# Performance work log

Measured on AMD Instinct MI355X. Metric: run time of the kernel, lower is better.

## Reference

```python
import jax, jax.numpy as jnp
import numpy as np

NUM_NODES = 1_000_000
H_DIM = 64
OUT_DIM = 32
NUM_RELS = 64
NUM_BASES = 4
N_SRC0 = 400_000
N_DST1 = 100_000
N_DST2 = 20_000
E1 = 600_000
E2 = 300_000


def setup_inputs() -> dict:
    key = jax.random.key(0)
    ks = jax.random.split(key, 16)
    inp = {
        "input_nodes": jax.random.randint(ks[0], (N_SRC0,), 0, NUM_NODES),
        "src1": jax.random.randint(ks[1], (E1,), 0, N_SRC0),
        "dst1": jax.random.randint(ks[2], (E1,), 0, N_DST1),
        "etype1": jax.random.randint(ks[3], (E1,), 0, NUM_RELS),
        "norm1": jax.random.uniform(ks[4], (E1, 1), dtype=jnp.float32),
        "src2": jax.random.randint(ks[5], (E2,), 0, N_DST1),
        "dst2": jax.random.randint(ks[6], (E2,), 0, N_DST2),
        "etype2": jax.random.randint(ks[7], (E2,), 0, NUM_RELS),
        "norm2": jax.random.uniform(ks[8], (E2, 1), dtype=jnp.float32),
        # learned parameters
        "emb": jax.random.normal(ks[9], (NUM_NODES, H_DIM), dtype=jnp.float32),
        "V1": jax.random.normal(ks[10], (NUM_BASES, H_DIM, H_DIM), dtype=jnp.float32) * 0.05,
        "comp1": jax.random.normal(ks[11], (NUM_RELS, NUM_BASES), dtype=jnp.float32) * 0.3,
        "b1": jnp.zeros((H_DIM,), dtype=jnp.float32),
        "V2": jax.random.normal(ks[12], (NUM_BASES, H_DIM, OUT_DIM), dtype=jnp.float32) * 0.05,
        "comp2": jax.random.normal(ks[13], (NUM_RELS, NUM_BASES), dtype=jnp.float32) * 0.3,
        "b2": jnp.zeros((OUT_DIM,), dtype=jnp.float32),
    }
    return inp


def rel_graph_conv(x, src, dst, etype, norm, V, comp, bias, n_dst):
    """Basis-decomposed RelGraphConv (no self-loop): m_e = (x[src_e] @ W_{etype_e}) * norm_e,
    with W_r = sum_b comp[r,b] V[b]; aggregate by sum into dst nodes, then add bias."""
    xe = x[src]                                 # [E, d] gather of source features
    coeff = comp[etype]                         # [E, B] relation coefficients per edge
    y = jnp.einsum('ed,bdo->ebo', xe, V)        # [E, B, o] feature x each basis
    m = jnp.einsum('ebo,eb->eo', y, coeff)      # [E, o] relation-specific message
    m = m * norm                                # per-edge normalization ([E,1] broadcast)
    h = jax.ops.segment_sum(m, dst, num_segments=n_dst)  # scatter-add to dst
    return h + bias


def reference(input_nodes, src1, dst1, etype1, norm1, src2, dst2, etype2, norm2,
              emb, V1, comp1, b1, V2, comp2, b2):
    x = emb[input_nodes]                                           # [N_src0, h]
    h = rel_graph_conv(x, src1, dst1, etype1, norm1, V1, comp1, b1, N_DST1)
    h = jax.nn.relu(h)
    out = rel_graph_conv(h, src2, dst2, etype2, norm2, V2, comp2, b2, N_DST2)
    return out
```

## Files before the change

kernel.cpp:

```cpp
#include <hip/hip_runtime.h>
#include <stdint.h>

#define NUM_NODES 1000000
#define H_DIM 64
#define OUT_DIM 32
#define NUM_RELS 64
#define NUM_BASES 4
#define N_SRC0 400000
#define N_DST1 100000
#define N_DST2 20000
#define E1 600000
#define E2 300000
#define NDST_TOT (N_DST1 + N_DST2)
#define E_TOT (E1 + E2)

typedef __attribute__((ext_vector_type(8))) short bf16x8;
typedef __attribute__((ext_vector_type(4))) float floatx4;

__device__ __forceinline__ unsigned short f2bf(float f){
  union{float f; unsigned u;} v; v.f=f;
  unsigned u=v.u;
  unsigned r=(u + 0x7FFFu + ((u>>16)&1u))>>16;
  return (unsigned short)r;
}
__device__ __forceinline__ float bf2f(unsigned short h){
  union{unsigned u; float f;} v; v.u=((unsigned)h)<<16; return v.f;
}

__global__ void k_init(const float* __restrict__ V1, const float* __restrict__ V2,
                       ushort* __restrict__ Btab1, ushort* __restrict__ Btab2,
                       int* __restrict__ deg){
  int t = blockIdx.x*blockDim.x + threadIdx.x;
  if (t < NDST_TOT) deg[t] = 0;
  if (t < 16384){
    int j = t & 7, lane = (t>>3)&63, kk = (t>>9)&7, nt = t>>12;
    int kdim = kk*32 + (lane>>4)*8 + j;
    int o = nt*16 + (lane&15);
    int k = kdim>>2, b = kdim&3;
    Btab1[t] = f2bf(V1[(b*64 + k)*64 + o]);
  } else if (t < 24576){
    int u = t - 16384;
    int j = u & 7, lane = (u>>3)&63, kk = (u>>9)&7, nt = u>>12;
    int kdim = kk*32 + (lane>>4)*8 + j;
    int o = nt*16 + (lane&15);
    int k = kdim>>2, b = kdim&3;
    Btab2[u] = f2bf(V2[(b*64 + k)*32 + o]);
  }
}

__global__ void k_hist(const int* __restrict__ dst1, const int* __restrict__ dst2,
                       int* __restrict__ deg){
  int t = blockIdx.x*blockDim.x + threadIdx.x;
  if (t < E1) atomicAdd(&deg[dst1[t]], 1);
  else if (t < E_TOT) atomicAdd(&deg[N_DST1 + dst2[t - E1]], 1);
}

__global__ void k_scan_sum(const int* __restrict__ deg, int* __restrict__ bsum, int n){
  __shared__ int lds[256];
  int tid = threadIdx.x;
  int base = blockIdx.x*1024 + tid*4;
  int s = 0;
  #pragma unroll
  for (int j=0;j<4;j++){ int i = base+j; if (i<n) s += deg[i]; }
  lds[tid] = s; __syncthreads();
  for (int off=128; off>0; off>>=1){ if (tid<off) lds[tid] += lds[tid+off]; __syncthreads(); }
  if (tid==0) bsum[blockIdx.x] = lds[0];
}

__global__ void k_scan_bsum(const int* __restrict__ bsum, int* __restrict__ boff, int nb){
  __shared__ int lds[256];
  int tid = threadIdx.x;
  int v = (tid<nb) ? bsum[tid] : 0;
  lds[tid] = v; __syncthreads();
  for (int off=1; off<256; off<<=1){
    int t = (tid>=off) ? lds[tid-off] : 0; __syncthreads();
    lds[tid] += t; __syncthreads();
  }
  if (tid<nb) boff[tid] = lds[tid] - v;
}

__global__ void k_scan_final(const int* __restrict__ deg, const int* __restrict__ boff,
                             int* __restrict__ offs, int* __restrict__ cursor, int n){
  __shared__ int lds[256];
  int tid = threadIdx.x;
  int base = blockIdx.x*1024 + tid*4;
  int a[4]; int s = 0;
  #pragma unroll
  for (int j=0;j<4;j++){ int i = base+j; a[j] = (i<n)?deg[i]:0; s += a[j]; }
  lds[tid] = s; __syncthreads();
  for (int off=1; off<256; off<<=1){
    int t = (tid>=off) ? lds[tid-off] : 0; __syncthreads();
    lds[tid] += t; __syncthreads();
  }
  int run = boff[blockIdx.x] + (lds[tid] - s);
  #pragma unroll
  for (int j=0;j<4;j++){
    int i = base+j;
    if (i<n){
      offs[i] = run; cursor[i] = run;
      run += a[j];
      if (i == n-1) offs[n] = run;
    }
  }
}

__global__ void k_scatter(const int* __restrict__ input_nodes,
                          const int* __restrict__ src1, const int* __restrict__ dst1,
                          const int* __restrict__ ety1, const float* __restrict__ nrm1,
                          const float* __restrict__ comp1,
                          const int* __restrict__ src2, const int* __restrict__ dst2,
                          const int* __restrict__ ety2, const float* __restrict__ nrm2,
                          const float* __restrict__ comp2,
                          int* __restrict__ cursor, int* __restrict__ ssrc,
                          float4* __restrict__ sc){
  int t = blockIdx.x*blockDim.x + threadIdx.x;
  int d, s, et; float nv; const float* comp;
  if (t < E1){
    d = dst1[t]; s = input_nodes[src1[t]]; et = ety1[t]; nv = nrm1[t]; comp = comp1;
  } else if (t < E_TOT){
    int e = t - E1;
    d = N_DST1 + dst2[e]; s = src2[e]; et = ety2[e]; nv = nrm2[e]; comp = comp2;
  } else return;
  int p = atomicAdd(&cursor[d], 1);
  ssrc[p] = s;
  float4 cp = ((const float4*)comp)[et];
  float4 c; c.x = cp.x*nv; c.y = cp.y*nv; c.z = cp.z*nv; c.w = cp.w*nv;
  sc[p] = c;
}


__global__ __launch_bounds__(1024) void k_agg_gemm1(
    const float* __restrict__ emb, const int* __restrict__ offs,
    const int* __restrict__ ssrc, const float4* __restrict__ sc,
    const ushort* __restrict__ Btab, const float* __restrict__ bias,
    ushort* __restrict__ h_bf){
  __shared__ ushort zt[16][264];
  int lane = threadIdx.x & 63;
  int w = threadIdx.x >> 6;
  int mbase = blockIdx.x * 16;
  int d = mbase + w;
  int e0 = offs[d], e1 = offs[d+1];
  float a0=0.f, a1=0.f, a2=0.f, a3=0.f;
  int elast = e1 - 1;
  for (int e = e0; e < e1; e += 4){
    int i0 = e,            i1 = min(e+1, elast);
    int i2 = min(e+2, elast), i3 = min(e+3, elast);
    int s0 = ssrc[i0], s1 = ssrc[i1], s2 = ssrc[i2], s3 = ssrc[i3];
    float4 c0 = sc[i0], c1 = sc[i1], c2 = sc[i2], c3 = sc[i3];
    if (e+1 > elast){ c1.x=0.f;c1.y=0.f;c1.z=0.f;c1.w=0.f; }
    if (e+2 > elast){ c2.x=0.f;c2.y=0.f;c2.z=0.f;c2.w=0.f; }
    if (e+3 > elast){ c3.x=0.f;c3.y=0.f;c3.z=0.f;c3.w=0.f; }
    float x0 = emb[(size_t)s0*64 + lane];
    float x1 = emb[(size_t)s1*64 + lane];
    float x2 = emb[(size_t)s2*64 + lane];
    float x3 = emb[(size_t)s3*64 + lane];
    a0 = fmaf(c0.x, x0, a0); a1 = fmaf(c0.y, x0, a1);
    a2 = fmaf(c0.z, x0, a2); a3 = fmaf(c0.w, x0, a3);
    a0 = fmaf(c1.x, x1, a0); a1 = fmaf(c1.y, x1, a1);
    a2 = fmaf(c1.z, x1, a2); a3 = fmaf(c1.w, x1, a3);
    a0 = fmaf(c2.x, x2, a0); a1 = fmaf(c2.y, x2, a1);
    a2 = fmaf(c2.z, x2, a2); a3 = fmaf(c2.w, x2, a3);
    a0 = fmaf(c3.x, x3, a0); a1 = fmaf(c3.y, x3, a1);
    a2 = fmaf(c3.z, x3, a2); a3 = fmaf(c3.w, x3, a3);
  }
  ushort4 o; o.x=f2bf(a0); o.y=f2bf(a1); o.z=f2bf(a2); o.w=f2bf(a3);
  *(ushort4*)&zt[w][lane*4] = o;
  __syncthreads();
  if (w >= 4) return;
  int quad = lane>>4, l15 = lane&15;
  bf16x8 a[8];
  #pragma unroll
  for (int kk=0; kk<8; kk++)
    a[kk] = *(const bf16x8*)&zt[l15][kk*32 + quad*8];
  floatx4 acc = {0.f,0.f,0.f,0.f};
  #pragma unroll
  for (int kk=0; kk<8; kk++){
    bf16x8 b = *((const bf16x8*)(Btab + ((w*8 + kk)*64 + lane)*8));
    acc = __builtin_amdgcn_mfma_f32_16x16x32_bf16(a[kk], b, acc, 0, 0, 0);
  }
  int col = w*16 + l15;
  float bv = bias[col];
  #pragma unroll
  for (int r=0; r<4; r++){
    int row = mbase + quad*4 + r;
    float v = fmaxf(acc[r] + bv, 0.f);
    h_bf[(size_t)row*64 + col] = f2bf(v);
  }
}

__global__ __launch_bounds__(1024) void k_agg_gemm2(
    const ushort* __restrict__ hin, const int* __restrict__ offs,
    const int* __restrict__ ssrc, const float4* __restrict__ sc,
    const ushort* __restrict__ Btab, const float* __restrict__ bias,
    float* __restrict__ out){
  __shared__ ushort zt[16][264];
  int lane = threadIdx.x & 63;
  int w = threadIdx.x >> 6;
  int mbase = blockIdx.x * 16;
  int d = mbase + w;
  int e0 = offs[d], e1 = offs[d+1];
  float a0=0.f, a1=0.f, a2=0.f, a3=0.f;
  int elast = e1 - 1;
  for (int e = e0; e < e1; e += 4){
    int i0 = e,            i1 = min(e+1, elast);
    int i2 = min(e+2, elast), i3 = min(e+3, elast);
    int s0 = ssrc[i0], s1 = ssrc[i1], s2 = ssrc[i2], s3 = ssrc[i3];
    float4 c0 = sc[i0], c1 = sc[i1], c2 = sc[i2], c3 = sc[i3];
    if (e+1 > elast){ c1.x=0.f;c1.y=0.f;c1.z=0.f;c1.w=0.f; }
    if (e+2 > elast){ c2.x=0.f;c2.y=0.f;c2.z=0.f;c2.w=0.f; }
    if (e+3 > elast){ c3.x=0.f;c3.y=0.f;c3.z=0.f;c3.w=0.f; }
    float x0 = bf2f(hin[(size_t)s0*64 + lane]);
    float x1 = bf2f(hin[(size_t)s1*64 + lane]);
    float x2 = bf2f(hin[(size_t)s2*64 + lane]);
    float x3 = bf2f(hin[(size_t)s3*64 + lane]);
    a0 = fmaf(c0.x, x0, a0); a1 = fmaf(c0.y, x0, a1);
    a2 = fmaf(c0.z, x0, a2); a3 = fmaf(c0.w, x0, a3);
    a0 = fmaf(c1.x, x1, a0); a1 = fmaf(c1.y, x1, a1);
    a2 = fmaf(c1.z, x1, a2); a3 = fmaf(c1.w, x1, a3);
    a0 = fmaf(c2.x, x2, a0); a1 = fmaf(c2.y, x2, a1);
    a2 = fmaf(c2.z, x2, a2); a3 = fmaf(c2.w, x2, a3);
    a0 = fmaf(c3.x, x3, a0); a1 = fmaf(c3.y, x3, a1);
    a2 = fmaf(c3.z, x3, a2); a3 = fmaf(c3.w, x3, a3);
  }
  ushort4 o; o.x=f2bf(a0); o.y=f2bf(a1); o.z=f2bf(a2); o.w=f2bf(a3);
  *(ushort4*)&zt[w][lane*4] = o;
  __syncthreads();
  if (w >= 2) return;
  int quad = lane>>4, l15 = lane&15;
  bf16x8 a[8];
  #pragma unroll
  for (int kk=0; kk<8; kk++)
    a[kk] = *(const bf16x8*)&zt[l15][kk*32 + quad*8];
  floatx4 acc = {0.f,0.f,0.f,0.f};
  #pragma unroll
  for (int kk=0; kk<8; kk++){
    bf16x8 b = *((const bf16x8*)(Btab + ((w*8 + kk)*64 + lane)*8));
    acc = __builtin_amdgcn_mfma_f32_16x16x32_bf16(a[kk], b, acc, 0, 0, 0);
  }
  int col = w*16 + l15;
  float bv = bias[col];
  #pragma unroll
  for (int r=0; r<4; r++){
    int row = mbase + quad*4 + r;
    out[(size_t)row*32 + col] = acc[r] + bv;
  }
}

extern "C" void kernel_launch(void* const* d_in, const int* in_sizes, int n_in,
                              void* d_out, int out_size, void* d_ws, size_t ws_size,
                              hipStream_t stream){
  const int*   input_nodes = (const int*)  d_in[0];
  const int*   src1  = (const int*)  d_in[1];
  const int*   dst1  = (const int*)  d_in[2];
  const int*   ety1  = (const int*)  d_in[3];
  const float* norm1 = (const float*)d_in[4];
  const int*   src2  = (const int*)  d_in[5];
  const int*   dst2  = (const int*)  d_in[6];
  const int*   ety2  = (const int*)  d_in[7];
  const float* norm2 = (const float*)d_in[8];
  const float* emb   = (const float*)d_in[9];
  const float* V1    = (const float*)d_in[10];
  const float* comp1 = (const float*)d_in[11];
  const float* b1    = (const float*)d_in[12];
  const float* V2    = (const float*)d_in[13];
  const float* comp2 = (const float*)d_in[14];
  const float* b2    = (const float*)d_in[15];
  float* out = (float*)d_out;

  char* p = (char*)d_ws;
  auto alloc = [&](size_t bytes)->char*{
    char* r = p; p += (bytes + 255) & ~(size_t)255; return r;
  };
  ushort* h_bf  = (ushort*)alloc((size_t)N_DST1*64*2);
  ushort* Btab1 = (ushort*)alloc(16384*2);
  ushort* Btab2 = (ushort*)alloc(8192*2);
  int* deg  = (int*)alloc((size_t)NDST_TOT*4);
  int* cur  = (int*)alloc((size_t)NDST_TOT*4);
  int* offs = (int*)alloc((size_t)(NDST_TOT+1)*4);
  int* bs   = (int*)alloc(256*4);
  int* bo   = (int*)alloc(256*4);
  int* ssrc = (int*)alloc((size_t)E_TOT*4);
  float4* sc = (float4*)alloc((size_t)E_TOT*16);

  k_init<<<(NDST_TOT + 255)/256, 256, 0, stream>>>(V1, V2, Btab1, Btab2, deg);
  k_hist<<<(E_TOT + 255)/256, 256, 0, stream>>>(dst1, dst2, deg);
  int nb = (NDST_TOT + 1023)/1024;
  k_scan_sum<<<nb, 256, 0, stream>>>(deg, bs, NDST_TOT);
  k_scan_bsum<<<1, 256, 0, stream>>>(bs, bo, nb);
  k_scan_final<<<nb, 256, 0, stream>>>(deg, bo, offs, cur, NDST_TOT);
  k_scatter<<<(E_TOT + 255)/256, 256, 0, stream>>>(input_nodes,
                                                   src1, dst1, ety1, norm1, comp1,
                                                   src2, dst2, ety2, norm2, comp2,
                                                   cur, ssrc, sc);
  k_agg_gemm1<<<N_DST1/16, 1024, 0, stream>>>(emb, offs, ssrc, sc, Btab1, b1, h_bf);
  k_agg_gemm2<<<N_DST2/16, 1024, 0, stream>>>(h_bf, offs + N_DST1, ssrc, sc, Btab2, b2, out);

  (void)in_sizes; (void)n_in; (void)out_size; (void)ws_size;
}
```

Baseline: 506.9 us.

## Replace three-kernel prefix scan with atomic per-wave bucket allocation

Replaces the three-pass exact prefix scan over destination degrees with a single kernel: each wavefront scans its 64 degrees with shuffles and reserves a contiguous range from a global atomic counter. Buckets are no longer in destination order, so the aggregation kernels now compute each segment end as offset plus degree. The Btab conversion is folded into the histogram kernel and degree zeroing moves to a memset, cutting the launch count. The cost is a loss of edge-segment ordering by destination, which may reduce locality of ssrc/sc reads in the aggregation kernels.

```diff
diff --git a/kernel.cpp b/kernel.cpp
--- a/kernel.cpp
+++ b/kernel.cpp
@@ -27,11 +27,11 @@
   union{unsigned u; float f;} v; v.u=((unsigned)h)<<16; return v.f;
 }
 
-__global__ void k_init(const float* __restrict__ V1, const float* __restrict__ V2,
-                       ushort* __restrict__ Btab1, ushort* __restrict__ Btab2,
-                       int* __restrict__ deg){
+__global__ void k_btab_hist(const float* __restrict__ V1, const float* __restrict__ V2,
+                            ushort* __restrict__ Btab1, ushort* __restrict__ Btab2,
+                            const int* __restrict__ dst1, const int* __restrict__ dst2,
+                            int* __restrict__ deg){
   int t = blockIdx.x*blockDim.x + threadIdx.x;
-  if (t < NDST_TOT) deg[t] = 0;
   if (t < 16384){
     int j = t & 7, lane = (t>>3)&63, kk = (t>>9)&7, nt = t>>12;
     int kdim = kk*32 + (lane>>4)*8 + j;
@@ -46,61 +46,28 @@
     int k = kdim>>2, b = kdim&3;
     Btab2[u] = f2bf(V2[(b*64 + k)*32 + o]);
   }
-}
-
-__global__ void k_hist(const int* __restrict__ dst1, const int* __restrict__ dst2,
-                       int* __restrict__ deg){
-  int t = blockIdx.x*blockDim.x + threadIdx.x;
   if (t < E1) atomicAdd(&deg[dst1[t]], 1);
   else if (t < E_TOT) atomicAdd(&deg[N_DST1 + dst2[t - E1]], 1);
 }
 
-__global__ void k_scan_sum(const int* __restrict__ deg, int* __restrict__ bsum, int n){
-  __shared__ int lds[256];
-  int tid = threadIdx.x;
-  int base = blockIdx.x*1024 + tid*4;
-  int s = 0;
-  #pragma unroll
-  for (int j=0;j<4;j++){ int i = base+j; if (i<n) s += deg[i]; }
-  lds[tid] = s; __syncthreads();
-  for (int off=128; off>0; off>>=1){ if (tid<off) lds[tid] += lds[tid+off]; __syncthreads(); }
-  if (tid==0) bsum[blockIdx.x] = lds[0];
-}
-
-__global__ void k_scan_bsum(const int* __restrict__ bsum, int* __restrict__ boff, int nb){
-  __shared__ int lds[256];
-  int tid = threadIdx.x;
-  int v = (tid<nb) ? bsum[tid] : 0;
-  lds[tid] = v; __syncthreads();
-  for (int off=1; off<256; off<<=1){
-    int t = (tid>=off) ? lds[tid-off] : 0; __syncthreads();
-    lds[tid] += t; __syncthreads();
-  }
-  if (tid<nb) boff[tid] = lds[tid] - v;
-}
-
-__global__ void k_scan_final(const int* __restrict__ deg, const int* __restrict__ boff,
-                             int* __restrict__ offs, int* __restrict__ cursor, int n){
-  __shared__ int lds[256];
-  int tid = threadIdx.x;
-  int base = blockIdx.x*1024 + tid*4;
-  int a[4]; int s = 0;
-  #pragma unroll
-  for (int j=0;j<4;j++){ int i = base+j; a[j] = (i<n)?deg[i]:0; s += a[j]; }
-  lds[tid] = s; __syncthreads();
-  for (int off=1; off<256; off<<=1){
-    int t = (tid>=off) ? lds[tid-off] : 0; __syncthreads();
-    lds[tid] += t; __syncthreads();
-  }
-  int run = boff[blockIdx.x] + (lds[tid] - s);
-  #pragma unroll
-  for (int j=0;j<4;j++){
-    int i = base+j;
-    if (i<n){
-      offs[i] = run; cursor[i] = run;
-      run += a[j];
-      if (i == n-1) offs[n] = run;
-    }
+__global__ void k_alloc(const int* __restrict__ deg, int* __restrict__ offs,
+                        int* __restrict__ cursor, int* __restrict__ counter){
+  int t = blockIdx.x*blockDim.x + threadIdx.x;
+  int lane = threadIdx.x & 63;
+  int d = (t < NDST_TOT) ? deg[t] : 0;
+  int incl = d;
+  #pragma unroll
+  for (int off=1; off<64; off<<=1){
+    int v = __shfl_up(incl, off);
+    if (lane >= off) incl += v;
+  }
+  int total = __shfl(incl, 63);
+  int base = 0;
+  if (lane == 0 && total > 0) base = atomicAdd(counter, total);
+  base = __shfl(base, 0);
+  if (t < NDST_TOT){
+    int o = base + incl - d;
+    offs[t] = o; cursor[t] = o;
   }
 }
 
@@ -131,6 +98,7 @@
 
 __global__ __launch_bounds__(1024) void k_agg_gemm1(
     const float* __restrict__ emb, const int* __restrict__ offs,
+    const int* __restrict__ deg,
     const int* __restrict__ ssrc, const float4* __restrict__ sc,
     const ushort* __restrict__ Btab, const float* __restrict__ bias,
     ushort* __restrict__ h_bf){
@@ -139,11 +107,11 @@
   int w = threadIdx.x >> 6;
   int mbase = blockIdx.x * 16;
   int d = mbase + w;
-  int e0 = offs[d], e1 = offs[d+1];
+  int e0 = offs[d], e1 = e0 + deg[d];
   float a0=0.f, a1=0.f, a2=0.f, a3=0.f;
   int elast = e1 - 1;
   for (int e = e0; e < e1; e += 4){
-    int i0 = e,            i1 = min(e+1, elast);
+    int i0 = e,               i1 = min(e+1, elast);
     int i2 = min(e+2, elast), i3 = min(e+3, elast);
     int s0 = ssrc[i0], s1 = ssrc[i1], s2 = ssrc[i2], s3 = ssrc[i3];
     float4 c0 = sc[i0], c1 = sc[i1], c2 = sc[i2], c3 = sc[i3];
@@ -190,6 +158,7 @@
 
 __global__ __launch_bounds__(1024) void k_agg_gemm2(
     const ushort* __restrict__ hin, const int* __restrict__ offs,
+    const int* __restrict__ deg,
     const int* __restrict__ ssrc, const float4* __restrict__ sc,
     const ushort* __restrict__ Btab, const float* __restrict__ bias,
     float* __restrict__ out){
@@ -198,11 +167,11 @@
   int w = threadIdx.x >> 6;
   int mbase = blockIdx.x * 16;
   int d = mbase + w;
-  int e0 = offs[d], e1 = offs[d+1];
+  int e0 = offs[d], e1 = e0 + deg[d];
   float a0=0.f, a1=0.f, a2=0.f, a3=0.f;
   int elast = e1 - 1;
   for (int e = e0; e < e1; e += 4){
-    int i0 = e,            i1 = min(e+1, elast);
+    int i0 = e,               i1 = min(e+1, elast);
     int i2 = min(e+2, elast), i3 = min(e+3, elast);
     int s0 = ssrc[i0], s1 = ssrc[i1], s2 = ssrc[i2], s3 = ssrc[i3];
     float4 c0 = sc[i0], c1 = sc[i1], c2 = sc[i2], c3 = sc[i3];
@@ -274,26 +243,24 @@
   ushort* h_bf  = (ushort*)alloc((size_t)N_DST1*64*2);
   ushort* Btab1 = (ushort*)alloc(16384*2);
   ushort* Btab2 = (ushort*)alloc(8192*2);
-  int* deg  = (int*)alloc((size_t)NDST_TOT*4);
+  int* deg  = (int*)alloc((size_t)(NDST_TOT+1)*4);
   int* cur  = (int*)alloc((size_t)NDST_TOT*4);
-  int* offs = (int*)alloc((size_t)(NDST_TOT+1)*4);
-  int* bs   = (int*)alloc(256*4);
-  int* bo   = (int*)alloc(256*4);
+  int* offs = (int*)alloc((size_t)NDST_TOT*4);
   int* ssrc = (int*)alloc((size_t)E_TOT*4);
   float4* sc = (float4*)alloc((size_t)E_TOT*16);
-
-  k_init<<<(NDST_TOT + 255)/256, 256, 0, stream>>>(V1, V2, Btab1, Btab2, deg);
-  k_hist<<<(E_TOT + 255)/256, 256, 0, stream>>>(dst1, dst2, deg);
-  int nb = (NDST_TOT + 1023)/1024;
-  k_scan_sum<<<nb, 256, 0, stream>>>(deg, bs, NDST_TOT);
-  k_scan_bsum<<<1, 256, 0, stream>>>(bs, bo, nb);
-  k_scan_final<<<nb, 256, 0, stream>>>(deg, bo, offs, cur, NDST_TOT);
+  int* counter = deg + NDST_TOT;
+
+  (void)hipMemsetAsync(deg, 0, (size_t)(NDST_TOT+1)*4, stream);
+  k_btab_hist<<<(E_TOT + 255)/256, 256, 0, stream>>>(V1, V2, Btab1, Btab2,
+                                                     dst1, dst2, deg);
+  k_alloc<<<(NDST_TOT + 255)/256, 256, 0, stream>>>(deg, offs, cur, counter);
   k_scatter<<<(E_TOT + 255)/256, 256, 0, stream>>>(input_nodes,
                                                    src1, dst1, ety1, norm1, comp1,
                                                    src2, dst2, ety2, norm2, comp2,
                                                    cur, ssrc, sc);
-  k_agg_gemm1<<<N_DST1/16, 1024, 0, stream>>>(emb, offs, ssrc, sc, Btab1, b1, h_bf);
-  k_agg_gemm2<<<N_DST2/16, 1024, 0, stream>>>(h_bf, offs + N_DST1, ssrc, sc, Btab2, b2, out);
+  k_agg_gemm1<<<N_DST1/16, 1024, 0, stream>>>(emb, offs, deg, ssrc, sc, Btab1, b1, h_bf);
+  k_agg_gemm2<<<N_DST2/16, 1024, 0, stream>>>(h_bf, offs + N_DST1, deg + N_DST1,
+                                              ssrc, sc, Btab2, b2, out);
 
   (void)in_sizes; (void)n_in; (void)out_size; (void)ws_size;
 }
```

New measurement: 524.8 us. +3.5%, slower.
